# Kernel optimization log

Measured on AMD Instinct MI355X. Metric: run time of the kernel, lower is better.

## Reference

```python
import jax, jax.numpy as jnp
import numpy as np

WT_LEVELS = 3  # wavelet decomposition levels

def haar2d(x):
    # orthonormal 2D Haar: 2x2 block -> 4 sub-bands, each scaled by 1/2
    a = x[:, :, 0::2, 0::2]; b = x[:, :, 0::2, 1::2]
    c = x[:, :, 1::2, 0::2]; d = x[:, :, 1::2, 1::2]
    ll = (a + b + c + d) * 0.5
    lh = (a - b + c - d) * 0.5
    hl = (a + b - c - d) * 0.5
    hh = (a - b - c + d) * 0.5
    return jnp.stack([ll, lh, hl, hh], axis=2)  # [B,C,4,h,w]

def ihaar2d(co):
    # exact inverse of haar2d
    ll, lh, hl, hh = co[:, :, 0], co[:, :, 1], co[:, :, 2], co[:, :, 3]
    a = (ll + lh + hl + hh) * 0.5
    b = (ll - lh + hl - hh) * 0.5
    c = (ll + lh - hl - hh) * 0.5
    d = (ll - lh - hl + hh) * 0.5
    B, C, h, w = ll.shape
    top = jnp.stack([a, b], axis=-1).reshape(B, C, h, 2 * w)
    bot = jnp.stack([c, d], axis=-1).reshape(B, C, h, 2 * w)
    return jnp.stack([top, bot], axis=3).reshape(B, C, 2 * h, 2 * w)

def dwconv(x, w):
    # depthwise conv, stride 1, 'same' padding (matches torch padding='same', k=5)
    return jax.lax.conv_general_dilated(
        x, w, (1, 1), 'SAME',
        dimension_numbers=('NCHW', 'OIHW', 'NCHW'),
        feature_group_count=x.shape[1])

def setup_inputs() -> dict:
    key = jax.random.key(0)
    ks = jax.random.split(key, 5)
    B, C, H, W, K, L = 8, 96, 224, 224, 5, WT_LEVELS
    x = jax.random.normal(ks[0], (B, C, H, W), jnp.float32)
    base_w = jax.random.normal(ks[1], (C, 1, K, K), jnp.float32) * 0.1
    base_b = jax.random.normal(ks[2], (C,), jnp.float32) * 0.01
    base_scale = jnp.ones((1, C, 1, 1), jnp.float32)
    wconv_w = jax.random.normal(ks[3], (L, 4 * C, 1, K, K), jnp.float32) * 0.1
    wscale = jnp.full((L, 1, 4 * C, 1, 1), 0.1, jnp.float32)
    return {"x": x, "base_w": base_w, "base_b": base_b,
            "base_scale": base_scale, "wconv_w": wconv_w, "wscale": wscale}

def reference(x, base_w, base_b, base_scale, wconv_w, wscale):
    B, C, H, W = x.shape
    # analysis cascade: decompose LL of previous level, conv+scale all 4 bands
    cur = x
    level_coeffs = []
    for i in range(WT_LEVELS):
        co = haar2d(cur)                 # [B,C,4,h,w]
        cur = co[:, :, 0]                # pre-conv LL feeds next level
        h, w = co.shape[-2:]
        flat = co.reshape(B, C * 4, h, w)
        flat = dwconv(flat, wconv_w[i]) * wscale[i]
        level_coeffs.append(flat.reshape(B, C, 4, h, w))
    # synthesis cascade: reconstructed LL from deeper level is added to
    # the shallower level's (convolved) LL band before inverse transform
    next_ll = jnp.zeros_like(level_coeffs[-1][:, :, 0])
    for i in reversed(range(WT_LEVELS)):
        co = level_coeffs[i].at[:, :, 0].add(next_ll)
        next_ll = ihaar2d(co)
    base = dwconv(x, base_w) * base_scale + base_b.reshape(1, C, 1, 1)
    return base + next_ll
```

## Files before the change

kernel.cpp:

```cpp
#include <hip/hip_runtime.h>

#define BB 8
#define CC 96
#define HH 224
#define WW 224

typedef _Float16 h2 __attribute__((ext_vector_type(2)));
__device__ __forceinline__ h2 u2h(unsigned u) { return __builtin_bit_cast(h2, u); }
__device__ __forceinline__ unsigned pkrtz(float a, float b) {
    return __builtin_bit_cast(unsigned, __builtin_amdgcn_cvt_pkrtz(a, b));
}

#if __has_builtin(__builtin_amdgcn_fdot2)
#define FDOT2(a, b, c) __builtin_amdgcn_fdot2((a), (b), (c), false)
#else
#define FDOT2(a, b, c) ((float)(a).x * (float)(b).x + (float)(a).y * (float)(b).y + (c))
#endif

__global__ __launch_bounds__(512, 4) void levels_fused2(
    const float* __restrict__ x,
    unsigned* __restrict__ rec1g,
    const float* __restrict__ wt1, const float* __restrict__ ws1,
    const float* __restrict__ wt2, const float* __restrict__ ws2)
{
    const int bc = blockIdx.x, c = bc % CC;
    const int t = threadIdx.x;

    __shared__ unsigned s_c1[112 * 58];
    __shared__ unsigned s_sb1[4 * 60 * 31];
    __shared__ unsigned s_cur2[56 * 30];
    __shared__ unsigned s_sb2[4 * 32 * 17];
    __shared__ unsigned s_w2[240];

    unsigned* const c1_01 = s_c1;
    unsigned* const c1_23 = s_c1 + 3192;
    unsigned* const c2_01 = s_cur2;
    unsigned* const c2_23 = s_cur2 + 812;
    float*    const rec2  = reinterpret_cast<float*>(s_sb1);

    for (int i = t; i < 4 * 60 * 31; i += 512) s_sb1[i] = 0;
    for (int i = t; i < 4 * 32 * 17; i += 512) s_sb2[i] = 0;

    if (t < 80) {
        int knl = t / 10;
        int par = t & 1, row = (t % 10) >> 1;
        int lvl = knl >> 2, s = knl & 3;
        const float* wt  = lvl ? wt2 : wt1;
        const float* wsc = lvl ? ws2 : ws1;
        float sc = 0.5f * wsc[c * 4 + s];
        float wv[5];
        #pragma unroll
        for (int j = 0; j < 5; ++j) wv[j] = wt[(c * 4 + s) * 25 + row * 5 + j] * sc;
        unsigned* dst = &s_w2[(knl * 2 + par) * 15 + row * 3];
        if (par == 0) {
            dst[0] = pkrtz(wv[0], wv[1]);
            dst[1] = pkrtz(wv[2], wv[3]);
            dst[2] = pkrtz(wv[4], 0.f);
        } else {
            dst[0] = pkrtz(0.f, wv[0]);
            dst[1] = pkrtz(wv[1], wv[2]);
            dst[2] = pkrtz(wv[3], wv[4]);
        }
    }

    const float* xp = x + (size_t)bc * HH * WW;
    for (int idx = t; idx < 112 * 56; idx += 512) {
        int r = idx / 56, g = idx % 56;
        const float* r0 = xp + (size_t)(2 * r) * WW + 4 * g;
        const float* r1 = r0 + WW;
        float4 a = *(const float4*)r0;
        float4 b = *(const float4*)r1;
        s_c1[r * 58 + g] = pkrtz(0.5f * (a.x + a.y + b.x + b.y),
                                 0.5f * (a.z + a.w + b.z + b.w));
    }
    __syncthreads();

    for (int idx = t; idx < 56 * 28; idx += 512) {
        int sr = idx / 28, sc2 = idx % 28;
        uint2 tp = *(const uint2*)&s_c1[(2 * sr) * 58 + 2 * sc2];
        uint2 bt = *(const uint2*)&s_c1[(2 * sr + 1) * 58 + 2 * sc2];
        h2 t0 = u2h(tp.x), t1 = u2h(tp.y), b0 = u2h(bt.x), b1 = u2h(bt.y);
        float P0 = (float)t0.x + (float)t0.y, M0 = (float)t0.x - (float)t0.y;
        float R0 = (float)b0.x + (float)b0.y, Q0 = (float)b0.x - (float)b0.y;
        float P1 = (float)t1.x + (float)t1.y, M1 = (float)t1.x - (float)t1.y;
        float R1 = (float)b1.x + (float)b1.y, Q1 = (float)b1.x - (float)b1.y;
        int o = (sr + 2) * 31 + (sc2 + 1);
        s_sb1[0 * 1860 + o] = pkrtz(P0 + R0, P1 + R1);
        s_sb1[1 * 1860 + o] = pkrtz(M0 + Q0, M1 + Q1);
        s_sb1[2 * 1860 + o] = pkrtz(P0 - R0, P1 - R1);
        s_sb1[3 * 1860 + o] = pkrtz(M0 - Q0, M1 - Q1);
        s_cur2[sr * 30 + sc2] = pkrtz(0.5f * (P0 + R0), 0.5f * (P1 + R1));
    }
    __syncthreads();

    if (t < 28 * 14) {
        int sr = t / 14, sc2 = t % 14;
        uint2 tp = *(const uint2*)&s_cur2[(2 * sr) * 30 + 2 * sc2];
        uint2 bt = *(const uint2*)&s_cur2[(2 * sr + 1) * 30 + 2 * sc2];
        h2 t0 = u2h(tp.x), t1 = u2h(tp.y), b0 = u2h(bt.x), b1 = u2h(bt.y);
        float P0 = (float)t0.x + (float)t0.y, M0 = (float)t0.x - (float)t0.y;
        float R0 = (float)b0.x + (float)b0.y, Q0 = (float)b0.x - (float)b0.y;
        float P1 = (float)t1.x + (float)t1.y, M1 = (float)t1.x - (float)t1.y;
        float R1 = (float)b1.x + (float)b1.y, Q1 = (float)b1.x - (float)b1.y;
        int o = (sr + 2) * 17 + (sc2 + 1);
        s_sb2[0 * 544 + o] = pkrtz(P0 + R0, P1 + R1);
        s_sb2[1 * 544 + o] = pkrtz(M0 + Q0, M1 + Q1);
        s_sb2[2 * 544 + o] = pkrtz(P0 - R0, P1 - R1);
        s_sb2[3 * 544 + o] = pkrtz(M0 - Q0, M1 - Q1);
    }

    {
        const int s = t >> 7, lane = t & 127;
        const int q = lane & 63, half = lane >> 6;
        if (q < 56) {
            const int par = q & 1, d0 = q >> 1, ps = half * 28;
            h2 w[5][3];
            {
                const unsigned* wp = &s_w2[(s * 2 + par) * 15];
                #pragma unroll
                for (int ki = 0; ki < 5; ++ki)
                    #pragma unroll
                    for (int m = 0; m < 3; ++m) w[ki][m] = u2h(wp[ki * 3 + m]);
            }
            float acc[28];
            #pragma unroll
            for (int r = 0; r < 28; ++r) acc[r] = 0.f;
            #pragma unroll
            for (int ri = 0; ri < 32; ++ri) {
                const unsigned* rp = &s_sb1[s * 1860 + (ps + ri) * 31 + d0];
                h2 g0 = u2h(rp[0]), g1 = u2h(rp[1]), g2 = u2h(rp[2]);
                #pragma unroll
                for (int ki = 0; ki < 5; ++ki) {
                    int r = ri - ki;
                    if (r >= 0 && r < 28)
                        acc[r] = FDOT2(g0, w[ki][0],
                                 FDOT2(g1, w[ki][1],
                                 FDOT2(g2, w[ki][2], acc[r])));
                }
            }
            _Float16* dstH = reinterpret_cast<_Float16*>((s < 2) ? c1_01 : c1_23);
            const int hf = s & 1;
            #pragma unroll
            for (int r = 0; r < 28; ++r)
                dstH[((ps + r) * 57 + q) * 2 + hf] = (_Float16)acc[r];
        }
    }
    __syncthreads();

    if (t < 112) {
        const int s = t / 28, q = t % 28;
        const int par = q & 1, d0 = q >> 1;
        h2 w[5][3];
        {
            const unsigned* wp = &s_w2[((4 + s) * 2 + par) * 15];
            #pragma unroll
            for (int ki = 0; ki < 5; ++ki)
                #pragma unroll
                for (int m = 0; m < 3; ++m) w[ki][m] = u2h(wp[ki * 3 + m]);
        }
        float acc[28];
        #pragma unroll
        for (int r = 0; r < 28; ++r) acc[r] = 0.f;
        #pragma unroll
        for (int ri = 0; ri < 32; ++ri) {
            const unsigned* rp = &s_sb2[s * 544 + ri * 17 + d0];
            h2 g0 = u2h(rp[0]), g1 = u2h(rp[1]), g2 = u2h(rp[2]);
            #pragma unroll
            for (int ki = 0; ki < 5; ++ki) {
                int r = ri - ki;
                if (r >= 0 && r < 28)
                    acc[r] = FDOT2(g0, w[ki][0],
                             FDOT2(g1, w[ki][1],
                             FDOT2(g2, w[ki][2], acc[r])));
            }
        }
        _Float16* dstH = reinterpret_cast<_Float16*>((s < 2) ? c2_01 : c2_23);
        const int hf = s & 1;
        #pragma unroll
        for (int r = 0; r < 28; ++r)
            dstH[(r * 29 + q) * 2 + hf] = (_Float16)acc[r];
    }
    __syncthreads();

    for (int i = t; i < 784; i += 512) {
        int p2 = i / 28, q2 = i % 28;
        h2 v01 = u2h(c2_01[p2 * 29 + q2]);
        h2 v23 = u2h(c2_23[p2 * 29 + q2]);
        float ll = v01.x, lh = v01.y, hl = v23.x, hh = v23.y;
        float a  = 0.5f * (ll + lh + hl + hh);
        float b  = 0.5f * (ll - lh + hl - hh);
        float cv = 0.5f * (ll + lh - hl - hh);
        float d  = 0.5f * (ll - lh - hl + hh);
        float* rp = &rec2[(2 * p2) * 57 + 2 * q2];
        rp[0] = a; rp[1] = b; rp[57] = cv; rp[58] = d;
    }
    __syncthreads();

    unsigned* rg = rec1g + (size_t)bc * 112 * 56;
    for (int i = t; i < 3136; i += 512) {
        int p1 = i / 56, q1 = i % 56;
        h2 v01 = u2h(c1_01[p1 * 57 + q1]);
        h2 v23 = u2h(c1_23[p1 * 57 + q1]);
        float ll = (float)v01.x + rec2[p1 * 57 + q1];
        float lh = v01.y, hl = v23.x, hh = v23.y;
        float a  = 0.5f * (ll + lh + hl + hh);
        float b  = 0.5f * (ll - lh + hl - hh);
        float cv = 0.5f * (ll + lh - hl - hh);
        float d  = 0.5f * (ll - lh - hl + hh);
        rg[(size_t)(2 * p1) * 56 + q1]     = pkrtz(a, cv) ;
        rg[(size_t)(2 * p1 + 1) * 56 + q1] = 0;
        rg[(size_t)(2 * p1) * 56 + q1]     = pkrtz(a, b);
        rg[(size_t)(2 * p1 + 1) * 56 + q1] = pkrtz(cv, d);
    }
}

__global__ __launch_bounds__(256, 7) void final_fused_v10(
    const float* __restrict__ x,
    const float* __restrict__ bw,
    const float* __restrict__ bb,
    const float* __restrict__ bs,
    const float* __restrict__ wt0,
    const float* __restrict__ wsc0,
    const unsigned* __restrict__ rec1g,
    float* __restrict__ out)
{
    const int bc = blockIdx.z, c = bc % CC;
    const int t = threadIdx.x;

    __shared__ unsigned s_x2[64 * 34];
    __shared__ unsigned s_sb[4 * 544];
    __shared__ float s_rec1[28 * 29];
    __shared__ unsigned s_w2[150];
    _Float16* const s_cvh = reinterpret_cast<_Float16*>(s_x2);

    if (t < 50) {
        int par = t & 1, row = (t >> 1) % 5, knl = t / 10;
        float wv[5];
        if (knl == 0) {
            float sc = bs[c];
            #pragma unroll
            for (int j = 0; j < 5; ++j) wv[j] = bw[c * 25 + row * 5 + j] * sc;
        } else {
            int s = knl - 1;
            float sc = 0.5f * wsc0[c * 4 + s];
            #pragma unroll
            for (int j = 0; j < 5; ++j) wv[j] = wt0[(c * 4 + s) * 25 + row * 5 + j] * sc;
        }
        unsigned* dst = &s_w2[((knl * 2 + par) * 5 + row) * 3];
        if (par == 0) {
            dst[0] = pkrtz(wv[0], wv[1]);
            dst[1] = pkrtz(wv[2], wv[3]);
            dst[2] = pkrtz(wv[4], 0.f);
        } else {
            dst[0] = pkrtz(0.f, wv[0]);
            dst[1] = pkrtz(wv[1], wv[2]);
            dst[2] = pkrtz(wv[3], wv[4]);
        }
    }

    if (t < 196) {
        #pragma unroll
        for (int k = 0; k < 2; ++k) {
            int idx = 2 * t + k;
            int r = idx / 14, d = idx % 14;
            unsigned v = rec1g[((size_t)bc * 112 + 28 * blockIdx.y + r) * 56
                               + 14 * blockIdx.x + d];
            h2 hv = u2h(v);
            s_rec1[r * 29 + 2 * d]     = hv.x;
            s_rec1[r * 29 + 2 * d + 1] = hv.y;
        }
    }

    const float* xp = x + (size_t)bc * HH * WW;
    const int gy0 = 56 * blockIdx.y - 4, gx0 = 56 * blockIdx.x - 4;
    for (int idx = t; idx < 1024; idx += 256) {
        int r = idx >> 4, j = idx & 15;
        int gr = gy0 + r, gc = gx0 + 4 * j;
        float4 v = make_float4(0.f, 0.f, 0.f, 0.f);
        if (gr >= 0 && gr < HH && gc >= 0 && gc + 3 < WW)
            v = *(const float4*)(xp + (size_t)gr * WW + gc);
        uint2 pp;
        pp.x = pkrtz(v.x, v.y);
        pp.y = pkrtz(v.z, v.w);
        *(uint2*)&s_x2[r * 34 + 2 * j] = pp;
    }
    __syncthreads();

    for (int idx = t; idx < 512; idx += 256) {
        int sr = idx >> 4, g = idx & 15;
        uint2 tp = *(const uint2*)&s_x2[(2 * sr) * 34 + 2 * g];
        uint2 bt = *(const uint2*)&s_x2[(2 * sr + 1) * 34 + 2 * g];
        h2 t0 = u2h(tp.x), t1 = u2h(tp.y), b0 = u2h(bt.x), b1 = u2h(bt.y);
        float a0 = t0.x, e0 = t0.y, cc0 = b0.x, f0 = b0.y;
        float a1 = t1.x, e1 = t1.y, cc1 = b1.x, f1 = b1.y;
        float P0 = a0 + e0, M0 = a0 - e0, R0 = cc0 + f0, Q0 = cc0 - f0;
        float P1 = a1 + e1, M1 = a1 - e1, R1 = cc1 + f1, Q1 = cc1 - f1;
        s_sb[0 * 544 + sr * 17 + g] = pkrtz(P0 + R0, P1 + R1);
        s_sb[1 * 544 + sr * 17 + g] = pkrtz(M0 + Q0, M1 + Q1);
        s_sb[2 * 544 + sr * 17 + g] = pkrtz(P0 - R0, P1 - R1);
        s_sb[3 * 544 + sr * 17 + g] = pkrtz(M0 - Q0, M1 - Q1);
    }

    const int q4 = t % 56, rb4 = t / 56;
    float bacc[14];
    if (t < 224) {
        const int par = q4 & 1, d0 = (q4 + 2) >> 1;
        h2 w[5][3];
        {
            const unsigned* wp = &s_w2[(par * 5) * 3];
            #pragma unroll
            for (int ki = 0; ki < 5; ++ki)
                #pragma unroll
                for (int m = 0; m < 3; ++m) w[ki][m] = u2h(wp[ki * 3 + m]);
        }
        #pragma unroll
        for (int r = 0; r < 14; ++r) bacc[r] = 0.f;
        #pragma unroll
        for (int ri = 0; ri < 18; ++ri) {
            const unsigned* rp = &s_x2[(rb4 * 14 + ri + 2) * 34 + d0];
            h2 g0 = u2h(rp[0]), g1 = u2h(rp[1]), g2 = u2h(rp[2]);
            #pragma unroll
            for (int ki = 0; ki < 5; ++ki) {
                int r = ri - ki;
                if (r >= 0 && r < 14)
                    bacc[r] = FDOT2(g0, w[ki][0],
                              FDOT2(g1, w[ki][1],
                              FDOT2(g2, w[ki][2], bacc[r])));
            }
        }
    }
    __syncthreads();

    {
        const int s = t >> 6, u = t & 63;
        if (u < 56) {
            const int q = u % 28, rb = u / 28;
            const int par = q & 1, d0 = q >> 1;
            h2 w[5][3];
            {
                const unsigned* wp = &s_w2[(((1 + s) * 2 + par) * 5) * 3];
                #pragma unroll
                for (int ki = 0; ki < 5; ++ki)
                    #pragma unroll
                    for (int m = 0; m < 3; ++m) w[ki][m] = u2h(wp[ki * 3 + m]);
            }
            float acc[14];
            #pragma unroll
            for (int r = 0; r < 14; ++r) acc[r] = 0.f;
            #pragma unroll
            for (int ri = 0; ri < 18; ++ri) {
                const unsigned* rp = &s_sb[s * 544 + (rb * 14 + ri) * 17 + d0];
                h2 g0 = u2h(rp[0]), g1 = u2h(rp[1]), g2 = u2h(rp[2]);
                #pragma unroll
                for (int ki = 0; ki < 5; ++ki) {
                    int r = ri - ki;
                    if (r >= 0 && r < 14)
                        acc[r] = FDOT2(g0, w[ki][0],
                                 FDOT2(g1, w[ki][1],
                                 FDOT2(g2, w[ki][2], acc[r])));
                }
            }
            #pragma unroll
            for (int r = 0; r < 14; ++r)
                s_cvh[(s * 28 + rb * 14 + r) * 29 + q] = (_Float16)acc[r];
        }
    }
    __syncthreads();

    if (t < 224) {
        const float bbv = bb[c];
        const int qs = q4 >> 1;
        const float sx = (q4 & 1) ? -1.f : 1.f;
        float* op = out + ((size_t)bc * HH + 56 * blockIdx.y + rb4 * 14) * WW
                        + 56 * blockIdx.x + q4;
        #pragma unroll
        for (int j = 0; j < 7; ++j) {
            const int p = rb4 * 7 + j;
            float ll = (float)s_cvh[(0 * 28 + p) * 29 + qs] + s_rec1[p * 29 + qs];
            float lh = (float)s_cvh[(1 * 28 + p) * 29 + qs];
            float hl = (float)s_cvh[(2 * 28 + p) * 29 + qs];
            float hh = (float)s_cvh[(3 * 28 + p) * 29 + qs];
            float e0 = ll + sx * lh;
            float e1 = hl + sx * hh;
            float top = 0.5f * (e0 + e1);
            float bot = 0.5f * (e0 - e1);
            op[(size_t)(2 * j) * WW]     = bacc[2 * j]     + bbv + top;
            op[(size_t)(2 * j + 1) * WW] = bacc[2 * j + 1] + bbv + bot;
        }
    }
}

extern "C" void kernel_launch(void* const* d_in, const int* in_sizes, int n_in,
                              void* d_out, int out_size, void* d_ws, size_t ws_size,
                              hipStream_t stream) {
    const float* x          = (const float*)d_in[0];
    const float* base_w     = (const float*)d_in[1];
    const float* base_b     = (const float*)d_in[2];
    const float* base_scale = (const float*)d_in[3];
    const float* wconv_w    = (const float*)d_in[4];
    const float* wscale     = (const float*)d_in[5];
    float* out = (float*)d_out;
    unsigned* rec1 = (unsigned*)d_ws;

    const int z = BB * CC;

    levels_fused2<<<z, 512, 0, stream>>>(
        x, rec1,
        wconv_w + 1 * 384 * 25, wscale + 1 * 384,
        wconv_w + 2 * 384 * 25, wscale + 2 * 384);
    final_fused_v10<<<dim3(4, 4, z), 256, 0, stream>>>(
        x, base_w, base_b, base_scale,
        wconv_w + 0 * 384 * 25, wscale + 0 * 384, rec1, out);
}
```

Measured before the change: 130.5 us.

## Rewrite final level kernel to compute depthwise convolutions with MFMA instructions

Replaces the fdot2-based 5x5 depthwise convolutions in the final kernel with 16x16x32 f16 MFMA ops, using banded Toeplitz weight fragments built per lane. Tiles change from 56x56 blocks to full-width 32-row strips (grid 7 x B*C), with a staged LDS epilogue that does the inverse Haar and writes float2 outputs. It also removes two redundant global stores in the first kernel. Trades extra zero-padded MFMA work, LDS zeroing and lower occupancy (launch bounds 3) for matrix-core throughput.

```diff
diff --git a/kernel.cpp b/kernel.cpp
--- a/kernel.cpp
+++ b/kernel.cpp
@@ -6,6 +6,8 @@
 #define WW 224
 
 typedef _Float16 h2 __attribute__((ext_vector_type(2)));
+typedef _Float16 v8h __attribute__((ext_vector_type(8)));
+typedef float v4f __attribute__((ext_vector_type(4)));
 __device__ __forceinline__ h2 u2h(unsigned u) { return __builtin_bit_cast(h2, u); }
 __device__ __forceinline__ unsigned pkrtz(float a, float b) {
     return __builtin_bit_cast(unsigned, __builtin_amdgcn_cvt_pkrtz(a, b));
@@ -207,14 +209,12 @@
         float b  = 0.5f * (ll - lh + hl - hh);
         float cv = 0.5f * (ll + lh - hl - hh);
         float d  = 0.5f * (ll - lh - hl + hh);
-        rg[(size_t)(2 * p1) * 56 + q1]     = pkrtz(a, cv) ;
-        rg[(size_t)(2 * p1 + 1) * 56 + q1] = 0;
         rg[(size_t)(2 * p1) * 56 + q1]     = pkrtz(a, b);
         rg[(size_t)(2 * p1 + 1) * 56 + q1] = pkrtz(cv, d);
     }
 }
 
-__global__ __launch_bounds__(256, 7) void final_fused_v10(
+__global__ __launch_bounds__(256, 3) void final_mfma(
     const float* __restrict__ x,
     const float* __restrict__ bw,
     const float* __restrict__ bb,
@@ -224,168 +224,175 @@
     const unsigned* __restrict__ rec1g,
     float* __restrict__ out)
 {
-    const int bc = blockIdx.z, c = bc % CC;
+    const int sy = blockIdx.x;
+    const int bc = blockIdx.y, c = bc % CC;
     const int t = threadIdx.x;
-
-    __shared__ unsigned s_x2[64 * 34];
-    __shared__ unsigned s_sb[4 * 544];
-    __shared__ float s_rec1[28 * 29];
-    __shared__ unsigned s_w2[150];
-    _Float16* const s_cvh = reinterpret_cast<_Float16*>(s_x2);
-
-    if (t < 50) {
-        int par = t & 1, row = (t >> 1) % 5, knl = t / 10;
-        float wv[5];
-        if (knl == 0) {
-            float sc = bs[c];
-            #pragma unroll
-            for (int j = 0; j < 5; ++j) wv[j] = bw[c * 25 + row * 5 + j] * sc;
-        } else {
-            int s = knl - 1;
-            float sc = 0.5f * wsc0[c * 4 + s];
-            #pragma unroll
-            for (int j = 0; j < 5; ++j) wv[j] = wt0[(c * 4 + s) * 25 + row * 5 + j] * sc;
-        }
-        unsigned* dst = &s_w2[((knl * 2 + par) * 5 + row) * 3];
-        if (par == 0) {
-            dst[0] = pkrtz(wv[0], wv[1]);
-            dst[1] = pkrtz(wv[2], wv[3]);
-            dst[2] = pkrtz(wv[4], 0.f);
-        } else {
-            dst[0] = pkrtz(0.f, wv[0]);
-            dst[1] = pkrtz(wv[1], wv[2]);
-            dst[2] = pkrtz(wv[3], wv[4]);
-        }
-    }
-
-    if (t < 196) {
-        #pragma unroll
-        for (int k = 0; k < 2; ++k) {
-            int idx = 2 * t + k;
-            int r = idx / 14, d = idx % 14;
-            unsigned v = rec1g[((size_t)bc * 112 + 28 * blockIdx.y + r) * 56
-                               + 14 * blockIdx.x + d];
-            h2 hv = u2h(v);
-            s_rec1[r * 29 + 2 * d]     = hv.x;
-            s_rec1[r * 29 + 2 * d + 1] = hv.y;
-        }
+    const int lane = t & 63, w = t >> 6;
+
+    __shared__ unsigned s_x[40 * 122];
+    __shared__ unsigned s_sb[4 * 20 * 66];
+    __shared__ unsigned s_rec[16 * 57];
+    __shared__ float s_wb[25];
+    __shared__ float s_ws[4 * 25];
+    unsigned* const cv01 = s_x;
+    unsigned* const cv23 = s_x + 16 * 113;
+    unsigned* const s_bc = s_sb;
+
+    for (int i = t; i < 40 * 122; i += 256) s_x[i] = 0;
+    for (int i = t; i < 4 * 20 * 66; i += 256) s_sb[i] = 0;
+
+    if (t < 25) s_wb[t] = bw[c * 25 + t] * bs[c];
+    if (t >= 32 && t < 132) {
+        int s = (t - 32) / 25, k = (t - 32) % 25;
+        s_ws[s * 25 + k] = wt0[(c * 4 + s) * 25 + k] * 0.5f * wsc0[c * 4 + s];
+    }
+
+    for (int idx = t; idx < 896; idx += 256) {
+        int r = idx / 56, d = idx % 56;
+        s_rec[r * 57 + d] = rec1g[((size_t)bc * 112 + 16 * sy + r) * 56 + d];
     }
 
     const float* xp = x + (size_t)bc * HH * WW;
-    const int gy0 = 56 * blockIdx.y - 4, gx0 = 56 * blockIdx.x - 4;
-    for (int idx = t; idx < 1024; idx += 256) {
-        int r = idx >> 4, j = idx & 15;
-        int gr = gy0 + r, gc = gx0 + 4 * j;
-        float4 v = make_float4(0.f, 0.f, 0.f, 0.f);
-        if (gr >= 0 && gr < HH && gc >= 0 && gc + 3 < WW)
-            v = *(const float4*)(xp + (size_t)gr * WW + gc);
-        uint2 pp;
-        pp.x = pkrtz(v.x, v.y);
-        pp.y = pkrtz(v.z, v.w);
-        *(uint2*)&s_x2[r * 34 + 2 * j] = pp;
-    }
-    __syncthreads();
-
-    for (int idx = t; idx < 512; idx += 256) {
-        int sr = idx >> 4, g = idx & 15;
-        uint2 tp = *(const uint2*)&s_x2[(2 * sr) * 34 + 2 * g];
-        uint2 bt = *(const uint2*)&s_x2[(2 * sr + 1) * 34 + 2 * g];
-        h2 t0 = u2h(tp.x), t1 = u2h(tp.y), b0 = u2h(bt.x), b1 = u2h(bt.y);
-        float a0 = t0.x, e0 = t0.y, cc0 = b0.x, f0 = b0.y;
-        float a1 = t1.x, e1 = t1.y, cc1 = b1.x, f1 = b1.y;
-        float P0 = a0 + e0, M0 = a0 - e0, R0 = cc0 + f0, Q0 = cc0 - f0;
-        float P1 = a1 + e1, M1 = a1 - e1, R1 = cc1 + f1, Q1 = cc1 - f1;
-        s_sb[0 * 544 + sr * 17 + g] = pkrtz(P0 + R0, P1 + R1);
-        s_sb[1 * 544 + sr * 17 + g] = pkrtz(M0 + Q0, M1 + Q1);
-        s_sb[2 * 544 + sr * 17 + g] = pkrtz(P0 - R0, P1 - R1);
-        s_sb[3 * 544 + sr * 17 + g] = pkrtz(M0 - Q0, M1 - Q1);
-    }
-
-    const int q4 = t % 56, rb4 = t / 56;
-    float bacc[14];
-    if (t < 224) {
-        const int par = q4 & 1, d0 = (q4 + 2) >> 1;
-        h2 w[5][3];
-        {
-            const unsigned* wp = &s_w2[(par * 5) * 3];
-            #pragma unroll
-            for (int ki = 0; ki < 5; ++ki)
-                #pragma unroll
-                for (int m = 0; m < 3; ++m) w[ki][m] = u2h(wp[ki * 3 + m]);
-        }
-        #pragma unroll
-        for (int r = 0; r < 14; ++r) bacc[r] = 0.f;
-        #pragma unroll
-        for (int ri = 0; ri < 18; ++ri) {
-            const unsigned* rp = &s_x2[(rb4 * 14 + ri + 2) * 34 + d0];
-            h2 g0 = u2h(rp[0]), g1 = u2h(rp[1]), g2 = u2h(rp[2]);
+    for (int idx = t; idx < 2240; idx += 256) {
+        int r = idx / 56, f = idx % 56;
+        int gr = 32 * sy - 4 + r;
+        if ((unsigned)gr < HH) {
+            float4 v = *(const float4*)(xp + (size_t)gr * WW + 4 * f);
+            unsigned* dp = &s_x[r * 122 + 2 * f + 3];
+            dp[0] = pkrtz(v.x, v.y);
+            dp[1] = pkrtz(v.z, v.w);
+        }
+    }
+    __syncthreads();
+
+    for (int idx = t; idx < 1160; idx += 256) {
+        int pp = idx / 58, q2 = idx % 58;
+        const unsigned* r0p = &s_x[(2 * pp) * 122 + 2 * q2 + 1];
+        const unsigned* r1p = &s_x[(2 * pp + 1) * 122 + 2 * q2 + 1];
+        h2 t0 = u2h(r0p[0]), t1 = u2h(r0p[1]);
+        h2 b0 = u2h(r1p[0]), b1 = u2h(r1p[1]);
+        float P0 = (float)t0.x + (float)t0.y, M0 = (float)t0.x - (float)t0.y;
+        float R0 = (float)b0.x + (float)b0.y, Q0 = (float)b0.x - (float)b0.y;
+        float P1 = (float)t1.x + (float)t1.y, M1 = (float)t1.x - (float)t1.y;
+        float R1 = (float)b1.x + (float)b1.y, Q1 = (float)b1.x - (float)b1.y;
+        int o = pp * 66 + q2;
+        s_sb[0 * 1320 + o] = pkrtz(P0 + R0, P1 + R1);
+        s_sb[1 * 1320 + o] = pkrtz(M0 + Q0, M1 + Q1);
+        s_sb[2 * 1320 + o] = pkrtz(P0 - R0, P1 - R1);
+        s_sb[3 * 1320 + o] = pkrtz(M0 - Q0, M1 - Q1);
+    }
+
+    const int nB = lane & 15, hB = lane >> 4;
+    v4f bcc[7];
+    {
+        v8h bfr[5];
+        #pragma unroll
+        for (int ki = 0; ki < 5; ++ki) {
+            v8h f;
+            #pragma unroll
+            for (int j = 0; j < 8; ++j) {
+                int d = 8 * hB + j - nB;
+                f[j] = (_Float16)((d >= 0 && d < 5) ? s_wb[ki * 5 + d] : 0.f);
+            }
+            bfr[ki] = f;
+        }
+        const int rt = w >> 1;
+        #pragma unroll
+        for (int i = 0; i < 7; ++i) {
+            int ct = (w & 1) * 7 + i;
+            v4f acc = {0.f, 0.f, 0.f, 0.f};
             #pragma unroll
             for (int ki = 0; ki < 5; ++ki) {
-                int r = ri - ki;
-                if (r >= 0 && r < 14)
-                    bacc[r] = FDOT2(g0, w[ki][0],
-                              FDOT2(g1, w[ki][1],
-                              FDOT2(g2, w[ki][2], bacc[r])));
-            }
-        }
-    }
-    __syncthreads();
-
+                int arow = rt * 16 + ki + nB + 2;
+                const unsigned* ap = &s_x[arow * 122 + 8 * ct + 2 + 4 * hB];
+                uint2 lo = *(const uint2*)ap;
+                uint2 hi = *(const uint2*)(ap + 2);
+                union { uint2 u2[2]; v8h v; } cvt;
+                cvt.u2[0] = lo; cvt.u2[1] = hi;
+                acc = __builtin_amdgcn_mfma_f32_16x16x32_f16(cvt.v, bfr[ki], acc, 0, 0, 0);
+            }
+            bcc[i] = acc;
+        }
+    }
+    __syncthreads();
+
+    v4f scc[7];
     {
-        const int s = t >> 6, u = t & 63;
-        if (u < 56) {
-            const int q = u % 28, rb = u / 28;
-            const int par = q & 1, d0 = q >> 1;
-            h2 w[5][3];
-            {
-                const unsigned* wp = &s_w2[(((1 + s) * 2 + par) * 5) * 3];
-                #pragma unroll
-                for (int ki = 0; ki < 5; ++ki)
-                    #pragma unroll
-                    for (int m = 0; m < 3; ++m) w[ki][m] = u2h(wp[ki * 3 + m]);
-            }
-            float acc[14];
-            #pragma unroll
-            for (int r = 0; r < 14; ++r) acc[r] = 0.f;
-            #pragma unroll
-            for (int ri = 0; ri < 18; ++ri) {
-                const unsigned* rp = &s_sb[s * 544 + (rb * 14 + ri) * 17 + d0];
-                h2 g0 = u2h(rp[0]), g1 = u2h(rp[1]), g2 = u2h(rp[2]);
-                #pragma unroll
-                for (int ki = 0; ki < 5; ++ki) {
-                    int r = ri - ki;
-                    if (r >= 0 && r < 14)
-                        acc[r] = FDOT2(g0, w[ki][0],
-                                 FDOT2(g1, w[ki][1],
-                                 FDOT2(g2, w[ki][2], acc[r])));
-                }
-            }
-            #pragma unroll
-            for (int r = 0; r < 14; ++r)
-                s_cvh[(s * 28 + rb * 14 + r) * 29 + q] = (_Float16)acc[r];
-        }
-    }
-    __syncthreads();
-
-    if (t < 224) {
+        v8h sfr[5];
+        #pragma unroll
+        for (int ki = 0; ki < 5; ++ki) {
+            v8h f;
+            #pragma unroll
+            for (int j = 0; j < 8; ++j) {
+                int d = 8 * hB + j - nB;
+                f[j] = (_Float16)((d >= 0 && d < 5) ? s_ws[w * 25 + ki * 5 + d] : 0.f);
+            }
+            sfr[ki] = f;
+        }
+        #pragma unroll
+        for (int i = 0; i < 7; ++i) {
+            v4f acc = {0.f, 0.f, 0.f, 0.f};
+            #pragma unroll
+            for (int ki = 0; ki < 5; ++ki) {
+                int arow = ki + nB;
+                const unsigned* ap = &s_sb[w * 1320 + arow * 66 + 8 * i + 4 * hB];
+                uint2 lo = *(const uint2*)ap;
+                uint2 hi = *(const uint2*)(ap + 2);
+                union { uint2 u2[2]; v8h v; } cvt;
+                cvt.u2[0] = lo; cvt.u2[1] = hi;
+                acc = __builtin_amdgcn_mfma_f32_16x16x32_f16(cvt.v, sfr[ki], acc, 0, 0, 0);
+            }
+            scc[i] = acc;
+        }
+    }
+    __syncthreads();
+
+    {
+        _Float16* bc16 = reinterpret_cast<_Float16*>(s_bc);
+        const int rt = w >> 1;
+        #pragma unroll
+        for (int i = 0; i < 7; ++i) {
+            int col = ((w & 1) * 7 + i) * 16 + nB;
+            #pragma unroll
+            for (int reg = 0; reg < 4; ++reg) {
+                int row = rt * 16 + 4 * hB + reg;
+                bc16[row * 226 + col] = (_Float16)bcc[i][reg];
+            }
+        }
+        _Float16* cv16 = reinterpret_cast<_Float16*>((w < 2) ? cv01 : cv23);
+        const int hf = w & 1;
+        #pragma unroll
+        for (int i = 0; i < 7; ++i) {
+            int col = i * 16 + nB;
+            #pragma unroll
+            for (int reg = 0; reg < 4; ++reg) {
+                int row = 4 * hB + reg;
+                cv16[(row * 113 + col) * 2 + hf] = (_Float16)scc[i][reg];
+            }
+        }
+    }
+    __syncthreads();
+
+    {
         const float bbv = bb[c];
-        const int qs = q4 >> 1;
-        const float sx = (q4 & 1) ? -1.f : 1.f;
-        float* op = out + ((size_t)bc * HH + 56 * blockIdx.y + rb4 * 14) * WW
-                        + 56 * blockIdx.x + q4;
-        #pragma unroll
-        for (int j = 0; j < 7; ++j) {
-            const int p = rb4 * 7 + j;
-            float ll = (float)s_cvh[(0 * 28 + p) * 29 + qs] + s_rec1[p * 29 + qs];
-            float lh = (float)s_cvh[(1 * 28 + p) * 29 + qs];
-            float hl = (float)s_cvh[(2 * 28 + p) * 29 + qs];
-            float hh = (float)s_cvh[(3 * 28 + p) * 29 + qs];
-            float e0 = ll + sx * lh;
-            float e1 = hl + sx * hh;
-            float top = 0.5f * (e0 + e1);
-            float bot = 0.5f * (e0 - e1);
-            op[(size_t)(2 * j) * WW]     = bacc[2 * j]     + bbv + top;
-            op[(size_t)(2 * j + 1) * WW] = bacc[2 * j + 1] + bbv + bot;
+        #pragma unroll
+        for (int it = 0; it < 7; ++it) {
+            int idx = t + it * 256;
+            int p = idx / 112, qq = idx % 112;
+            h2 v01 = u2h(cv01[p * 113 + qq]);
+            h2 v23 = u2h(cv23[p * 113 + qq]);
+            h2 rr  = u2h(s_rec[p * 57 + (qq >> 1)]);
+            float ll = (float)v01.x + (float)((qq & 1) ? rr.y : rr.x);
+            float lh = v01.y, hl = v23.x, hh = v23.y;
+            float a  = 0.5f * (ll + lh + hl + hh);
+            float b2 = 0.5f * (ll - lh + hl - hh);
+            float cv = 0.5f * (ll + lh - hl - hh);
+            float d  = 0.5f * (ll - lh - hl + hh);
+            h2 bt = u2h(s_bc[(2 * p) * 113 + qq]);
+            h2 bm = u2h(s_bc[(2 * p + 1) * 113 + qq]);
+            float* op = out + ((size_t)bc * HH + 32 * sy + 2 * p) * WW + 2 * qq;
+            *(float2*)op        = make_float2(a + (float)bt.x + bbv, b2 + (float)bt.y + bbv);
+            *(float2*)(op + WW) = make_float2(cv + (float)bm.x + bbv, d + (float)bm.y + bbv);
         }
     }
 }
@@ -408,7 +415,7 @@
         x, rec1,
         wconv_w + 1 * 384 * 25, wscale + 1 * 384,
         wconv_w + 2 * 384 * 25, wscale + 2 * 384);
-    final_fused_v10<<<dim3(4, 4, z), 256, 0, stream>>>(
+    final_mfma<<<dim3(7, z), 256, 0, stream>>>(
         x, base_w, base_b, base_scale,
         wconv_w + 0 * 384 * 25, wscale + 0 * 384, rec1, out);
 }
```

New measurement: 159.2 us. 22.0% more time.
